# Kernel optimization log

Hardware: AMD Instinct MI355X
Metric: run time of the kernel (lower is better)

The kernel has to match this reference:

```python
import jax, jax.numpy as jnp
import numpy as np

B, Z, H, T = 256, 512, 2048, 16
EPS = 1e-5

def _normalize(v):
    return v / (jnp.linalg.norm(v) + 1e-12)

def setup_inputs() -> dict:
    key = jax.random.key(0)
    ks = jax.random.split(key, 10)
    s = lambda fan: 1.0 / np.sqrt(fan)
    return {
        "z": jax.random.normal(ks[0], (B, Z), dtype=jnp.float32),
        "fc_w": jax.random.normal(ks[1], (Z, Z), dtype=jnp.float32) * s(Z),
        "fc_b": jnp.zeros((Z,), dtype=jnp.float32),
        "fc_u": _normalize(jax.random.normal(ks[2], (Z,), dtype=jnp.float32)),
        "w_ih": jax.random.normal(ks[3], (3 * H, Z), dtype=jnp.float32) * s(Z),
        "w_hh": jax.random.normal(ks[4], (3 * H, H), dtype=jnp.float32) * s(H),
        "b_ih": jnp.zeros((3 * H,), dtype=jnp.float32).at[H:2 * H].set(1.0),  # forget-gate bias init
        "b_hh": jnp.zeros((3 * H,), dtype=jnp.float32),
        "lin_w": jax.random.normal(ks[5], (Z, H), dtype=jnp.float32) * s(H),
        "lin_b": jnp.zeros((Z,), dtype=jnp.float32),
    }

def _spectral_norm(w, u):
    # one torch-style power iteration (u, v treated as constants)
    v = jax.lax.stop_gradient(_normalize(w.T @ u))
    u1 = jax.lax.stop_gradient(_normalize(w @ v))
    sigma = u1 @ (w @ v)
    return w / sigma

def reference(z, fc_w, fc_b, fc_u, w_ih, w_hh, b_ih, b_hh, lin_w, lin_b):
    # spectral-norm linear: h0 = z @ (W/sigma)^T + b
    w_sn = _spectral_norm(fc_w, fc_u)
    x0 = z @ w_sn.T + fc_b                      # [B, Z]
    h0 = jnp.zeros((B, H), dtype=z.dtype)       # initHidden

    def step(carry, _):
        x, h = carry
        gi = x @ w_ih.T + b_ih                  # [B, 3H]
        gh = h @ w_hh.T + b_hh                  # [B, 3H]
        i_r, i_z, i_n = jnp.split(gi, 3, axis=1)
        h_r, h_z, h_n = jnp.split(gh, 3, axis=1)
        r = jax.nn.sigmoid(i_r + h_r)
        u = jax.nn.sigmoid(i_z + h_z)
        n = jnp.tanh(i_n + r * h_n)
        h_new = (1.0 - u) * n + u * h
        x_new = h_new @ lin_w.T + lin_b         # [B, Z] fed back as next input
        return (x_new, h_new), x_new

    _, outs = jax.lax.scan(step, (x0, h0), None, length=T)  # [T, B, Z]

    # per-timestep BatchNorm1d(affine=False), training-mode batch stats
    mean = jnp.mean(outs, axis=1, keepdims=True)
    var = jnp.mean((outs - mean) ** 2, axis=1, keepdims=True)
    y = (outs - mean) / jnp.sqrt(var + EPS)     # [T, B, Z]

    y = jnp.transpose(y, (1, 0, 2))             # [B, T, Z]
    return y.reshape(-1, Z)                     # [B*T, Z]
```

## Files before the change

kernel.cpp:

```cpp
#include <hip/hip_runtime.h>
#include <hip/hip_bf16.h>
#include <cstdint>
#include <cstddef>

#define B_  256
#define Z_  512
#define H_  2048
#define T_  16
#define H3_ 6144

using short8  = __attribute__((ext_vector_type(8))) short;
using bf16x8  = __attribute__((ext_vector_type(8))) __bf16;
using f32x4   = __attribute__((ext_vector_type(4))) float;
using f32x16  = __attribute__((ext_vector_type(16))) float;

__device__ __forceinline__ f32x4 mfma_bf16(short8 a, short8 b, f32x4 c) {
  return __builtin_amdgcn_mfma_f32_16x16x32_bf16(
      __builtin_bit_cast(bf16x8, a), __builtin_bit_cast(bf16x8, b), c, 0, 0, 0);
}
__device__ __forceinline__ f32x16 mfma_bf16_32(short8 a, short8 b, f32x16 c) {
  return __builtin_amdgcn_mfma_f32_32x32x16_bf16(
      __builtin_bit_cast(bf16x8, a), __builtin_bit_cast(bf16x8, b), c, 0, 0, 0);
}

__device__ __forceinline__ unsigned short f2bf(float f) {
  unsigned int u = __builtin_bit_cast(unsigned int, f);
  u = (u + 0x7FFFu + ((u >> 16) & 1u)) >> 16;
  return (unsigned short)u;
}

__device__ __forceinline__ float sigmoidf_(float x) { return 1.0f / (1.0f + __expf(-x)); }

__device__ __forceinline__ int swz(int row, int chunk) {
  return row * 64 + ((chunk ^ (row & 7)) << 3);
}

__global__ __launch_bounds__(512, 1) void gru_step7(
    const unsigned short* __restrict__ A, int K,
    const unsigned short* __restrict__ Wr,
    const unsigned short* __restrict__ Wz,
    const unsigned short* __restrict__ Wn,
    const unsigned short* __restrict__ Whn,
    const float* __restrict__ cr, const float* __restrict__ cz,
    const float* __restrict__ cn, const float* __restrict__ chn,
    float hn_scale,
    const float* __restrict__ h_old,
    float* __restrict__ h_new,
    unsigned short* __restrict__ h_hist)
{
  __shared__ __align__(16) unsigned short sbuf[2][12288];
  __shared__ float red[6][4096];
  float* LDSf = (float*)sbuf;
  const int bid = blockIdx.x, tid = threadIdx.x;
  const int xcd = bid & 7, rst = bid >> 3;
  const int m_idx = rst & 3, gg = rst >> 2;
  const int grp = gg * 8 + xcd;
  const int m0 = m_idx * 64;
  const int gh0 = grp * 32;
  const int wave = tid >> 6, lane = tid & 63;
  const int s4 = wave & 3, gp = wave >> 2;
  const int lh = lane >> 5, l31 = lane & 31;

  const int arow = tid >> 3, achk = tid & 7;
  const int wrow = tid >> 2, wc0 = (tid & 3) * 2;
  const unsigned short* wsrc =
      (wrow < 32) ? Wr : (wrow < 64) ? Wz : (wrow < 96) ? Wn : Whn;
  const size_t aoff = (size_t)(m0 + arow) * K + achk * 8;
  const size_t woff = (size_t)(gh0 + (wrow & 31)) * K + wc0 * 8;
  const int sa_d  = swz(arow, achk);
  const int sw_d0 = 4096 + swz(wrow, wc0 + 0);
  const int sw_d1 = 4096 + swz(wrow, wc0 + 1);

  uint4 Aa, Aw0, Aw1;
  uint4 Ba, Bw0, Bw1;

#define LDSET(a, w0, w1, k0)                               \
  {                                                        \
    const int kk_ = (k0);                                  \
    a  = *(const uint4*)(A    + aoff + kk_);               \
    w0 = *(const uint4*)(wsrc + woff + kk_);               \
    w1 = *(const uint4*)(wsrc + woff + kk_ + 8);           \
  }
#define STAGE(s, a, w0, w1)                                \
  {                                                        \
    unsigned short* b_ = sbuf[s];                          \
    *(uint4*)(b_ + sa_d)  = a;                             \
    *(uint4*)(b_ + sw_d0) = w0;                            \
    *(uint4*)(b_ + sw_d1) = w1;                            \
  }

  f32x16 a00 = {}, a01 = {}, a10 = {}, a11 = {};
  const int g0r = gp * 64, g1r = gp * 64 + 32;

#define COMP(sb)                                                           \
  {                                                                        \
    const unsigned short* b_ = sbuf[sb];                                   \
    const int ch = s4 * 2 + lh;                                            \
    short8 af0 = *(const short8*)(b_ + swz(l31, ch));                      \
    short8 af1 = *(const short8*)(b_ + swz(32 + l31, ch));                 \
    short8 wf0 = *(const short8*)(b_ + 4096 + swz(g0r + l31, ch));         \
    short8 wf1 = *(const short8*)(b_ + 4096 + swz(g1r + l31, ch));         \
    a00 = mfma_bf16_32(af0, wf0, a00);                                     \
    a01 = mfma_bf16_32(af0, wf1, a01);                                     \
    a10 = mfma_bf16_32(af1, wf0, a10);                                     \
    a11 = mfma_bf16_32(af1, wf1, a11);                                     \
  }

  const int nIter = K >> 6;
  LDSET(Aa, Aw0, Aw1, 0);
  LDSET(Ba, Bw0, Bw1, 64);
  for (int it = 0; it < nIter; it += 2) {
    STAGE(0, Aa, Aw0, Aw1);
    __syncthreads();
    { const int kn = (it + 2 < nIter) ? ((it + 2) << 6) : 0;
      LDSET(Aa, Aw0, Aw1, kn); }
    COMP(0);
    STAGE(1, Ba, Bw0, Bw1);
    __syncthreads();
    { const int kn = (it + 3 < nIter) ? ((it + 3) << 6) : 64;
      LDSET(Ba, Bw0, Bw1, kn); }
    COMP(1);
  }
#undef LDSET
#undef STAGE
#undef COMP

  __syncthreads();
  if (s4 != 0) {
    float* rp = red[(s4 - 1) * 2 + gp];
#pragma unroll
    for (int r = 0; r < 16; ++r) rp[(0 * 16 + r) * 64 + lane] = a00[r];
#pragma unroll
    for (int r = 0; r < 16; ++r) rp[(1 * 16 + r) * 64 + lane] = a01[r];
#pragma unroll
    for (int r = 0; r < 16; ++r) rp[(2 * 16 + r) * 64 + lane] = a10[r];
#pragma unroll
    for (int r = 0; r < 16; ++r) rp[(3 * 16 + r) * 64 + lane] = a11[r];
  }
  __syncthreads();
  if (s4 == 0) {
#pragma unroll
    for (int ss = 0; ss < 3; ++ss) {
      const float* rp = red[ss * 2 + gp];
#pragma unroll
      for (int r = 0; r < 16; ++r) a00[r] += rp[(0 * 16 + r) * 64 + lane];
#pragma unroll
      for (int r = 0; r < 16; ++r) a01[r] += rp[(1 * 16 + r) * 64 + lane];
#pragma unroll
      for (int r = 0; r < 16; ++r) a10[r] += rp[(2 * 16 + r) * 64 + lane];
#pragma unroll
      for (int r = 0; r < 16; ++r) a11[r] += rp[(3 * 16 + r) * 64 + lane];
    }
    const int gA = gp * 2, gB = gp * 2 + 1;
#pragma unroll
    for (int r = 0; r < 16; ++r) {
      const int trow = (r & 3) + 8 * (r >> 2) + 4 * lh;
      LDSf[(gA * 64 + trow     ) * 33 + l31] = a00[r];
      LDSf[(gB * 64 + trow     ) * 33 + l31] = a01[r];
      LDSf[(gA * 64 + 32 + trow) * 33 + l31] = a10[r];
      LDSf[(gB * 64 + 32 + trow) * 33 + l31] = a11[r];
    }
  }
  __syncthreads();
  {
    const int row = tid >> 3, c0 = (tid & 7) * 4;
    const int grow = m0 + row;
#pragma unroll
    for (int j = 0; j < 4; ++j) {
      const int col = c0 + j;
      const int gcol = gh0 + col;
      const float R   = sigmoidf_(LDSf[(0 * 64 + row) * 33 + col] + cr[gcol]);
      const float U   = sigmoidf_(LDSf[(1 * 64 + row) * 33 + col] + cz[gcol]);
      const float HNv = hn_scale * LDSf[(3 * 64 + row) * 33 + col] + chn[gcol];
      const float Nv  = tanhf(LDSf[(2 * 64 + row) * 33 + col] + cn[gcol] + R * HNv);
      const float ho  = h_old ? h_old[(size_t)grow * H_ + gcol] : 0.0f;
      const float hv  = (1.0f - U) * Nv + U * ho;
      h_new[(size_t)grow * H_ + gcol]  = hv;
      h_hist[(size_t)grow * H_ + gcol] = f2bf(hv);
    }
  }
}

__global__ __launch_bounds__(512) void gemm128_wsum(
    const unsigned short* __restrict__ w_ih_q,
    const unsigned short* __restrict__ lin_wT_q,
    const float* __restrict__ w_hh,
    unsigned short* __restrict__ Wsum_r,
    unsigned short* __restrict__ Wsum_z,
    unsigned short* __restrict__ Wn_c)
{
  __shared__ __align__(16) unsigned short sA[2][8192];
  __shared__ __align__(16) unsigned short sB[2][8192];
  const int g = blockIdx.y >> 4, nj = blockIdx.y & 15;
  const unsigned short* Aq = w_ih_q + (size_t)g * H_ * Z_;
  const float* adds = (g < 2) ? (w_hh + (size_t)g * H_ * H_) : nullptr;
  unsigned short* outw = (g == 0) ? Wsum_r : (g == 1) ? Wsum_z : Wn_c;
  const int K = Z_;
  const int m0 = blockIdx.x * 128, n0 = nj * 128;
  const int tid = threadIdx.x;
  const int wave = tid >> 6, lane = tid & 63;
  const int wr = wave & 1, wc = wave >> 1;
  const int lh = lane >> 5, l31 = lane & 31;
  const int srow = tid >> 2, sc0 = (tid & 3) * 2;
  const size_t aoff = (size_t)(m0 + srow) * K + sc0 * 8;
  const size_t boff = (size_t)(n0 + srow) * K + sc0 * 8;
  const int sd0 = swz(srow, sc0), sd1 = swz(srow, sc0 + 1);
  f32x16 acc0 = {}, acc1 = {};
  uint4 A0, A1, B0, B1, C0, C1, D0, D1;
#define LD(a0, a1, b0, b1, k0)                              \
  { const int kk_ = (k0);                                   \
    a0 = *(const uint4*)(Aq + aoff + kk_);                  \
    a1 = *(const uint4*)(Aq + aoff + kk_ + 8);              \
    b0 = *(const uint4*)(lin_wT_q + boff + kk_);            \
    b1 = *(const uint4*)(lin_wT_q + boff + kk_ + 8); }
#define ST(s, a0, a1, b0, b1)                               \
  { *(uint4*)(sA[s] + sd0) = a0; *(uint4*)(sA[s] + sd1) = a1; \
    *(uint4*)(sB[s] + sd0) = b0; *(uint4*)(sB[s] + sd1) = b1; }
#define CP(s)                                               \
  { _Pragma("unroll")                                       \
    for (int ks = 0; ks < 4; ++ks) {                        \
      const int ch = ks * 2 + lh;                           \
      short8 af0 = *(const short8*)(sA[s] + swz(wr * 64 + l31, ch));      \
      short8 af1 = *(const short8*)(sA[s] + swz(wr * 64 + 32 + l31, ch)); \
      short8 bf  = *(const short8*)(sB[s] + swz(wc * 32 + l31, ch));      \
      acc0 = mfma_bf16_32(af0, bf, acc0);                   \
      acc1 = mfma_bf16_32(af1, bf, acc1); } }
  const int nIter = K >> 6;
  LD(A0, A1, B0, B1, 0);
  LD(C0, C1, D0, D1, 64);
  for (int it = 0; it < nIter; it += 2) {
    ST(0, A0, A1, B0, B1);
    __syncthreads();
    { const int kn = (it + 2 < nIter) ? ((it + 2) << 6) : 0; LD(A0, A1, B0, B1, kn); }
    CP(0);
    ST(1, C0, C1, D0, D1);
    __syncthreads();
    { const int kn = (it + 3 < nIter) ? ((it + 3) << 6) : 64; LD(C0, C1, D0, D1, kn); }
    CP(1);
  }
#undef LD
#undef ST
#undef CP
#pragma unroll
  for (int i = 0; i < 2; ++i) {
    const f32x16 a = i ? acc1 : acc0;
#pragma unroll
    for (int r = 0; r < 16; ++r) {
      const int row = m0 + wr * 64 + i * 32 + (r & 3) + 8 * (r >> 2) + 4 * lh;
      const int col = n0 + wc * 32 + l31;
      float val = a[r];
      if (adds) val += adds[(size_t)row * H_ + col];
      outw[(size_t)row * H_ + col] = f2bf(val);
    }
  }
}

__global__ __launch_bounds__(256) void gemm_bt(
    const unsigned short* __restrict__ A,
    const unsigned short* __restrict__ Bw,
    int K,
    const float* __restrict__ addsrc, int add_ld,
    const float* __restrict__ bias,
    const float* __restrict__ scale_ptr,
    unsigned short* __restrict__ out_bf,
    float* __restrict__ out_f, int ldo)
{
  __shared__ unsigned short sA[32 * 64];
  __shared__ unsigned short sB[64 * 64];
  const int tid  = threadIdx.x;
  const int m0   = blockIdx.x * 32, n0 = blockIdx.y * 64;
  const int wave = tid >> 6, lane = tid & 63;
  const int wr = wave & 1, wc = wave >> 1;
  const int q = lane >> 4, c16 = lane & 15;
  const int lr = tid >> 3, lc8 = tid & 7;
  f32x4 acc0 = {}, acc1 = {};
  const size_t rowA  = (size_t)(m0 + lr) * K;
  const size_t rowB0 = (size_t)(n0 + lr) * K;
  const size_t rowB1 = (size_t)(n0 + 32 + lr) * K;
  for (int k0 = 0; k0 < K; k0 += 64) {
    const int gc = k0 + lc8 * 8;
    uint4 ra  = *(const uint4*)(A  + rowA  + gc);
    uint4 rb0 = *(const uint4*)(Bw + rowB0 + gc);
    uint4 rb1 = *(const uint4*)(Bw + rowB1 + gc);
    __syncthreads();
    *(uint4*)(sA + swz(lr, lc8))      = ra;
    *(uint4*)(sB + swz(lr, lc8))      = rb0;
    *(uint4*)(sB + swz(32 + lr, lc8)) = rb1;
    __syncthreads();
#pragma unroll
    for (int kk = 0; kk < 2; ++kk) {
      const int arow = wr * 16 + c16;
      short8 af = *(const short8*)(sA + swz(arow, kk * 4 + q));
      const int brow = wc * 32 + c16;
      short8 b0 = *(const short8*)(sB + swz(brow, kk * 4 + q));
      acc0 = mfma_bf16(af, b0, acc0);
      short8 b1 = *(const short8*)(sB + swz(brow + 16, kk * 4 + q));
      acc1 = mfma_bf16(af, b1, acc1);
    }
  }
  const float scale = scale_ptr ? *scale_ptr : 1.0f;
#pragma unroll
  for (int cf = 0; cf < 2; ++cf) {
    f32x4 a = cf ? acc1 : acc0;
#pragma unroll
    for (int v = 0; v < 4; ++v) {
      const int row = m0 + wr * 16 + q * 4 + v;
      const int col = n0 + wc * 32 + cf * 16 + c16;
      float val = a[v] * scale;
      if (addsrc) val += addsrc[(size_t)row * add_ld + col];
      if (bias)   val += bias[col];
      if (out_f)  out_f[(size_t)row * ldo + col] = val;
      if (out_bf) out_bf[(size_t)row * ldo + col] = f2bf(val);
    }
  }
}

__global__ __launch_bounds__(256) void gemm_bt64(
    const unsigned short* __restrict__ A,
    const unsigned short* __restrict__ Bw,
    int K,
    const float* __restrict__ addsrc, int add_ld,
    const float* __restrict__ bias,
    unsigned short* __restrict__ out_bf,
    float* __restrict__ out_f, int ldo)
{
  __shared__ unsigned short sA[64 * 64];
  __shared__ unsigned short sB[64 * 64];
  const int tid  = threadIdx.x;
  const int m0   = blockIdx.x * 64, n0 = blockIdx.y * 64;
  const int wave = tid >> 6, lane = tid & 63;
  const int wr = wave & 1, wc = wave >> 1;
  const int q = lane >> 4, c16 = lane & 15;
  const int lr = tid >> 3, lc8 = tid & 7;
  f32x4 acc[2][2] = {};
  const size_t aoff = (size_t)(m0 + lr) * K;
  const size_t boff = (size_t)(n0 + lr) * K;
  const size_t s32  = (size_t)32 * K;

  uint4 ra0, ra1, rb0, rb1;
  auto LOAD = [&](int k0) {
    const int gc = k0 + lc8 * 8;
    ra0 = *(const uint4*)(A  + aoff + gc);
    ra1 = *(const uint4*)(A  + aoff + s32 + gc);
    rb0 = *(const uint4*)(Bw + boff + gc);
    rb1 = *(const uint4*)(Bw + boff + s32 + gc);
  };

  const int nIter = K >> 6;
  LOAD(0);
  for (int it = 0; it < nIter; ++it) {
    __syncthreads();
    *(uint4*)(sA + swz(lr, lc8))      = ra0;
    *(uint4*)(sA + swz(lr + 32, lc8)) = ra1;
    *(uint4*)(sB + swz(lr, lc8))      = rb0;
    *(uint4*)(sB + swz(lr + 32, lc8)) = rb1;
    __syncthreads();
    if (it + 1 < nIter) LOAD((it + 1) << 6);
#pragma unroll
    for (int kk = 0; kk < 2; ++kk) {
      short8 af0 = *(const short8*)(sA + swz(wr * 32 + c16,      kk * 4 + q));
      short8 af1 = *(const short8*)(sA + swz(wr * 32 + 16 + c16, kk * 4 + q));
      short8 bf0 = *(const short8*)(sB + swz(wc * 32 + c16,      kk * 4 + q));
      short8 bf1 = *(const short8*)(sB + swz(wc * 32 + 16 + c16, kk * 4 + q));
      acc[0][0] = mfma_bf16(af0, bf0, acc[0][0]);
      acc[0][1] = mfma_bf16(af0, bf1, acc[0][1]);
      acc[1][0] = mfma_bf16(af1, bf0, acc[1][0]);
      acc[1][1] = mfma_bf16(af1, bf1, acc[1][1]);
    }
  }
#pragma unroll
  for (int i = 0; i < 2; ++i) {
#pragma unroll
    for (int j = 0; j < 2; ++j) {
#pragma unroll
      for (int v = 0; v < 4; ++v) {
        const int row = m0 + wr * 32 + i * 16 + q * 4 + v;
        const int col = n0 + wc * 32 + j * 16 + c16;
        float val = acc[i][j][v];
        if (addsrc) val += addsrc[(size_t)row * add_ld + col];
        if (bias)   val += bias[col];
        if (out_f)  out_f[(size_t)row * ldo + col] = val;
        if (out_bf) out_bf[(size_t)row * ldo + col] = f2bf(val);
      }
    }
  }
}

__global__ __launch_bounds__(256) void quant_all(
    const float* __restrict__ z, const float* __restrict__ fc_w,
    const float* __restrict__ w_ih, const float* __restrict__ w_hh,
    const float* __restrict__ lin_w,
    unsigned short* __restrict__ z_q, unsigned short* __restrict__ fc_w_q,
    unsigned short* __restrict__ w_ih_q, unsigned short* __restrict__ w_hhn_q,
    unsigned short* __restrict__ lin_w_q)
{
  const int i = blockIdx.x * 256 + threadIdx.x;
  if (i >= 2195456) return;
  const float4* src; ushort4* dst; int idx;
  if (i < 32768)        { src = (const float4*)z;     dst = (ushort4*)z_q;     idx = i; }
  else if (i < 98304)   { src = (const float4*)fc_w;  dst = (ushort4*)fc_w_q;  idx = i - 32768; }
  else if (i < 884736)  { src = (const float4*)w_ih;  dst = (ushort4*)w_ih_q;  idx = i - 98304; }
  else if (i < 1933312) { src = (const float4*)(w_hh + (size_t)2 * H_ * H_);
                          dst = (ushort4*)w_hhn_q;    idx = i - 884736; }
  else                  { src = (const float4*)lin_w; dst = (ushort4*)lin_w_q; idx = i - 1933312; }
  float4 v = src[idx];
  ushort4 o; o.x = f2bf(v.x); o.y = f2bf(v.y); o.z = f2bf(v.z); o.w = f2bf(v.w);
  dst[idx] = o;
}

__global__ __launch_bounds__(256) void transq(const float* __restrict__ s,
                                              unsigned short* __restrict__ d) {
  __shared__ float tile[32][33];
  const int tx = threadIdx.x & 31, ty = threadIdx.x >> 5;
  const int k0 = blockIdx.x * 32, z0 = blockIdx.y * 32;
#pragma unroll
  for (int j = 0; j < 4; ++j)
    tile[ty + j * 8][tx] = s[(size_t)(z0 + ty + j * 8) * H_ + k0 + tx];
  __syncthreads();
#pragma unroll
  for (int j = 0; j < 4; ++j)
    d[(size_t)(k0 + ty + j * 8) * Z_ + z0 + tx] = f2bf(tile[tx][ty + j * 8]);
}

__global__ void sigma1(const float* __restrict__ W, const float* __restrict__ u,
                       float* __restrict__ t1) {
  __shared__ float part[4][64];
  const int lane = threadIdx.x & 63, wv = threadIdx.x >> 6;
  const int col = blockIdx.x * 64 + lane;
  float s = 0.f;
  for (int r = wv * 128; r < wv * 128 + 128; ++r)
    s += W[(size_t)r * Z_ + col] * u[r];
  part[wv][lane] = s;
  __syncthreads();
  if (wv == 0)
    t1[col] = part[0][lane] + part[1][lane] + part[2][lane] + part[3][lane];
}

__global__ void sigma2(const float* __restrict__ W, const float* __restrict__ t1,
                       float* __restrict__ t2) {
  __shared__ float red[256];
  const int tid = threadIdx.x;
  float p = 0.f;
  for (int c = tid; c < Z_; c += 256) { float v = t1[c]; p += v * v; }
  red[tid] = p;
  __syncthreads();
  for (int s = 128; s > 0; s >>= 1) {
    if (tid < s) red[tid] += red[tid + s];
    __syncthreads();
  }
  const float invn = 1.0f / (sqrtf(red[0]) + 1e-12f);
  const int lane = tid & 63, wv = tid >> 6;
  const int row = blockIdx.x * 4 + wv;
  float s = 0.f;
  for (int c = lane; c < Z_; c += 64) s += W[(size_t)row * Z_ + c] * t1[c];
#pragma unroll
  for (int off = 32; off > 0; off >>= 1) s += __shfl_down(s, off);
  if (lane == 0) t2[row] = s * invn;
}

__global__ void sigma3(const float* __restrict__ t2, float* __restrict__ inv_sig) {
  __shared__ float red[256];
  int t = threadIdx.x;
  float v0 = t2[t], v1 = t2[t + 256];
  red[t] = v0 * v0 + v1 * v1;
  __syncthreads();
  for (int s = 128; s > 0; s >>= 1) {
    if (t < s) red[t] += red[t + s];
    __syncthreads();
  }
  if (t == 0) {
    float s2  = red[0];
    float sig = s2 / (sqrtf(s2) + 1e-12f);
    inv_sig[0] = 1.0f / sig;
  }
}

__global__ __launch_bounds__(256) void dots2_k(
    const float* __restrict__ w, const float* __restrict__ lb,
    const float* __restrict__ b_ih, const float* __restrict__ b_hh,
    float* __restrict__ c0r, float* __restrict__ c0z, float* __restrict__ c0n,
    float* __restrict__ c1r, float* __restrict__ c1z, float* __restrict__ c1n,
    float* __restrict__ chn)
{
  const int wave = threadIdx.x >> 6, lane = threadIdx.x & 63;
#pragma unroll
  for (int i = 0; i < 4; ++i) {
    int row = blockIdx.x * 16 + wave * 4 + i;
    float s = 0.f;
    for (int c = lane; c < Z_; c += 64) s += w[(size_t)row * Z_ + c] * lb[c];
#pragma unroll
    for (int off = 32; off > 0; off >>= 1) s += __shfl_down(s, off);
    if (lane == 0) {
      const int g = row >> 11, j = row & 2047;
      const float bi = b_ih[row], bh = b_hh[row];
      if (g == 0)      { c0r[j] = bi + bh; c1r[j] = bi + bh + s; }
      else if (g == 1) { c0z[j] = bi + bh; c1z[j] = bi + bh + s; }
      else             { c0n[j] = bi;      c1n[j] = bi + s;      chn[j] = bh; }
    }
  }
}

__global__ __launch_bounds__(256) void bn_k(const float* __restrict__ outs,
                                            float* __restrict__ y) {
  __shared__ float s_sum[4][64], s_sq[4][64], s_mean[64], s_inv[64];
  const int t = blockIdx.x, zb = blockIdx.y;
  const int zl = threadIdx.x & 63, bp = threadIdx.x >> 6;
  const int z = zb * 64 + zl;
  float sum = 0.f, sq = 0.f;
  for (int b = bp * 64; b < bp * 64 + 64; ++b) {
    float v = outs[(size_t)(t * 256 + b) * Z_ + z];
    sum += v; sq += v * v;
  }
  s_sum[bp][zl] = sum; s_sq[bp][zl] = sq;
  __syncthreads();
  if (bp == 0) {
    float S = s_sum[0][zl] + s_sum[1][zl] + s_sum[2][zl] + s_sum[3][zl];
    float Q = s_sq[0][zl] + s_sq[1][zl] + s_sq[2][zl] + s_sq[3][zl];
    float mean = S * (1.0f / 256.0f);
    float var  = Q * (1.0f / 256.0f) - mean * mean;
    s_mean[zl] = mean;
    s_inv[zl]  = rsqrtf(var + 1e-5f);
  }
  __syncthreads();
  const float mean = s_mean[zl], inv = s_inv[zl];
  for (int b = bp * 64; b < bp * 64 + 64; ++b) {
    float v = outs[(size_t)(t * 256 + b) * Z_ + z];
    y[(size_t)(b * T_ + t) * Z_ + z] = (v - mean) * inv;
  }
}

extern "C" void kernel_launch(void* const* d_in, const int* in_sizes, int n_in,
                              void* d_out, int out_size, void* d_ws, size_t ws_size,
                              hipStream_t stream) {
  const float* z     = (const float*)d_in[0];
  const float* fc_w  = (const float*)d_in[1];
  const float* fc_b  = (const float*)d_in[2];
  const float* fc_u  = (const float*)d_in[3];
  const float* w_ih  = (const float*)d_in[4];
  const float* w_hh  = (const float*)d_in[5];
  const float* b_ih  = (const float*)d_in[6];
  const float* b_hh  = (const float*)d_in[7];
  const float* lin_w = (const float*)d_in[8];
  const float* lin_b = (const float*)d_in[9];
  float* out = (float*)d_out;

  char* ws = (char*)d_ws;
  size_t off = 0;
  auto alloc = [&](size_t bytes) -> void* {
    off = (off + 255) & ~(size_t)255;
    void* p = ws + off;
    off += bytes;
    return p;
  };
  unsigned short* w_ih_q   = (unsigned short*)alloc((size_t)H3_ * Z_ * 2);
  unsigned short* w_hhn_q  = (unsigned short*)alloc((size_t)H_ * H_ * 2);
  unsigned short* lin_w_q  = (unsigned short*)alloc((size_t)Z_ * H_ * 2);
  unsigned short* lin_wT_q = (unsigned short*)alloc((size_t)Z_ * H_ * 2);
  unsigned short* fc_w_q   = (unsigned short*)alloc((size_t)Z_ * Z_ * 2);
  unsigned short* z_q      = (unsigned short*)alloc((size_t)B_ * Z_ * 2);
  unsigned short* x0_q     = (unsigned short*)alloc((size_t)B_ * Z_ * 2);
  unsigned short* Wsum_r   = (unsigned short*)alloc((size_t)H_ * H_ * 2);
  unsigned short* Wsum_z   = (unsigned short*)alloc((size_t)H_ * H_ * 2);
  unsigned short* Wn_c     = (unsigned short*)alloc((size_t)H_ * H_ * 2);
  unsigned short* Hhist    = (unsigned short*)alloc((size_t)T_ * B_ * H_ * 2);
  float* h_f32 = (float*)alloc((size_t)2 * B_ * H_ * 4);
  float* outs  = (float*)alloc((size_t)T_ * B_ * Z_ * 4);
  float* c0r = (float*)alloc(H_ * 4);
  float* c0z = (float*)alloc(H_ * 4);
  float* c0n = (float*)alloc(H_ * 4);
  float* c1r = (float*)alloc(H_ * 4);
  float* c1z = (float*)alloc(H_ * 4);
  float* c1n = (float*)alloc(H_ * 4);
  float* chn = (float*)alloc(H_ * 4);
  float* t1v = (float*)alloc(Z_ * 4);
  float* t2v = (float*)alloc(Z_ * 4);
  float* invsig = (float*)alloc(256);
  (void)in_sizes; (void)n_in; (void)out_size; (void)ws_size;

  quant_all<<<dim3((2195456 + 255) / 256), 256, 0, stream>>>(
      z, fc_w, w_ih, w_hh, lin_w, z_q, fc_w_q, w_ih_q, w_hhn_q, lin_w_q);
  transq<<<dim3(64, 16), 256, 0, stream>>>(lin_w, lin_wT_q);
  sigma1<<<8, 256, 0, stream>>>(fc_w, fc_u, t1v);
  sigma2<<<128, 256, 0, stream>>>(fc_w, t1v, t2v);
  sigma3<<<1, 256, 0, stream>>>(t2v, invsig);
  dots2_k<<<384, 256, 0, stream>>>(w_ih, lin_b, b_ih, b_hh,
                                   c0r, c0z, c0n, c1r, c1z, c1n, chn);

  gemm_bt<<<dim3(B_ / 32, Z_ / 64), 256, 0, stream>>>(
      z_q, fc_w_q, Z_, nullptr, 0, fc_b, invsig, x0_q, nullptr, Z_);

  gemm128_wsum<<<dim3(H_ / 128, 48), 512, 0, stream>>>(
      w_ih_q, lin_wT_q, w_hh, Wsum_r, Wsum_z, Wn_c);

  for (int t = 0; t < T_; ++t) {
    if (t == 0) {
      gru_step7<<<256, 512, 0, stream>>>(
          x0_q, Z_,
          w_ih_q, w_ih_q + (size_t)H_ * Z_, w_ih_q + (size_t)2 * H_ * Z_,
          w_ih_q ,
          c0r, c0z, c0n, chn, 0.0f, nullptr, h_f32, Hhist);
    } else {
      gru_step7<<<256, 512, 0, stream>>>(
          Hhist + (size_t)(t - 1) * B_ * H_, H_,
          Wsum_r, Wsum_z, Wn_c, w_hhn_q,
          c1r, c1z, c1n, chn, 1.0f,
          h_f32 + (size_t)((t - 1) & 1) * B_ * H_,
          h_f32 + (size_t)(t & 1) * B_ * H_,
          Hhist + (size_t)t * B_ * H_);
    }
  }

  gemm_bt64<<<dim3(T_ * B_ / 64, Z_ / 64), 256, 0, stream>>>(
      Hhist, lin_w_q, H_, nullptr, 0, lin_b, nullptr, outs, Z_);

  bn_k<<<dim3(T_, Z_ / 64), 256, 0, stream>>>(outs, out);
}
```

Measured before the change: 411.4 us.

## Use direct global-to-LDS loads in GRU step and XCD-swizzle GEMM tiles

The per-step GRU kernel now loads A and weight tiles with global_load_lds straight into swizzled LDS. This replaces the register-staged double buffer with a single-sync-per-iteration pipeline, cutting VGPR traffic and LDS store instructions on the recurrent critical path. The W-sum precompute GEMM moves from a 128x128 32x32-MFMA kernel to a shared 64x64 core with an XCD-aware block remap, and the output GEMM gets the same remap for L2 locality. The new load path relies on the swizzle being built into the per-lane global addresses. A single barrier per iteration may expose load latency or cause overwrite races.

Result: slower. 530.0 us (+28.8%).

```diff
diff --git a/kernel.cpp b/kernel.cpp
--- a/kernel.cpp
+++ b/kernel.cpp
@@ -35,7 +35,13 @@
   return row * 64 + ((chunk ^ (row & 7)) << 3);
 }
 
-__global__ __launch_bounds__(512, 1) void gru_step7(
+__device__ __forceinline__ void gload16(const unsigned short* g, unsigned short* l) {
+  __builtin_amdgcn_global_load_lds(
+      (const __attribute__((address_space(1))) unsigned int*)g,
+      (__attribute__((address_space(3))) unsigned int*)l, 16, 0, 0);
+}
+
+__global__ __launch_bounds__(512, 1) void gru_step8(
     const unsigned short* __restrict__ A, int K,
     const unsigned short* __restrict__ Wr,
     const unsigned short* __restrict__ Wz,
@@ -61,37 +67,31 @@
   const int s4 = wave & 3, gp = wave >> 2;
   const int lh = lane >> 5, l31 = lane & 31;
 
-  const int arow = tid >> 3, achk = tid & 7;
-  const int wrow = tid >> 2, wc0 = (tid & 3) * 2;
+  const int lrow8 = lane >> 3;
+  const int csw = ((lane & 7) ^ lrow8) << 3;
+  const int arow = wave * 8 + lrow8;
+  const unsigned short* gA = A + (size_t)(m0 + arow) * K + csw;
+  const int wv2 = wave >> 1;
   const unsigned short* wsrc =
-      (wrow < 32) ? Wr : (wrow < 64) ? Wz : (wrow < 96) ? Wn : Whn;
-  const size_t aoff = (size_t)(m0 + arow) * K + achk * 8;
-  const size_t woff = (size_t)(gh0 + (wrow & 31)) * K + wc0 * 8;
-  const int sa_d  = swz(arow, achk);
-  const int sw_d0 = 4096 + swz(wrow, wc0 + 0);
-  const int sw_d1 = 4096 + swz(wrow, wc0 + 1);
-
-  uint4 Aa, Aw0, Aw1;
-  uint4 Ba, Bw0, Bw1;
-
-#define LDSET(a, w0, w1, k0)                               \
-  {                                                        \
-    const int kk_ = (k0);                                  \
-    a  = *(const uint4*)(A    + aoff + kk_);               \
-    w0 = *(const uint4*)(wsrc + woff + kk_);               \
-    w1 = *(const uint4*)(wsrc + woff + kk_ + 8);           \
-  }
-#define STAGE(s, a, w0, w1)                                \
+      (wv2 == 0) ? Wr : (wv2 == 1) ? Wz : (wv2 == 2) ? Wn : Whn;
+  const int wrow0 = (wave * 16 + lrow8) & 31;
+  const int wrow1 = (wave * 16 + 8 + lrow8) & 31;
+  const unsigned short* gW0 = wsrc + (size_t)(gh0 + wrow0) * K + csw;
+  const unsigned short* gW1 = wsrc + (size_t)(gh0 + wrow1) * K + csw;
+  const int ldsA  = wave * 512;
+  const int ldsW0 = 4096 + wave * 1024;
+  const int ldsW1 = 4096 + wave * 1024 + 512;
+
+  f32x16 a00 = {}, a01 = {}, a10 = {}, a11 = {};
+  const int g0r = gp * 64, g1r = gp * 64 + 32;
+
+#define ISSUE(s, k0)                                       \
   {                                                        \
     unsigned short* b_ = sbuf[s];                          \
-    *(uint4*)(b_ + sa_d)  = a;                             \
-    *(uint4*)(b_ + sw_d0) = w0;                            \
-    *(uint4*)(b_ + sw_d1) = w1;                            \
-  }
-
-  f32x16 a00 = {}, a01 = {}, a10 = {}, a11 = {};
-  const int g0r = gp * 64, g1r = gp * 64 + 32;
-
+    gload16(gA  + (k0), b_ + ldsA);                        \
+    gload16(gW0 + (k0), b_ + ldsW0);                       \
+    gload16(gW1 + (k0), b_ + ldsW1);                       \
+  }
 #define COMP(sb)                                                           \
   {                                                                        \
     const unsigned short* b_ = sbuf[sb];                                   \
@@ -107,25 +107,16 @@
   }
 
   const int nIter = K >> 6;
-  LDSET(Aa, Aw0, Aw1, 0);
-  LDSET(Ba, Bw0, Bw1, 64);
-  for (int it = 0; it < nIter; it += 2) {
-    STAGE(0, Aa, Aw0, Aw1);
-    __syncthreads();
-    { const int kn = (it + 2 < nIter) ? ((it + 2) << 6) : 0;
-      LDSET(Aa, Aw0, Aw1, kn); }
-    COMP(0);
-    STAGE(1, Ba, Bw0, Bw1);
-    __syncthreads();
-    { const int kn = (it + 3 < nIter) ? ((it + 3) << 6) : 64;
-      LDSET(Ba, Bw0, Bw1, kn); }
-    COMP(1);
-  }
-#undef LDSET
-#undef STAGE
+  ISSUE(0, 0);
+  __syncthreads();
+  for (int it = 0; it < nIter; ++it) {
+    if (it + 1 < nIter) ISSUE((it + 1) & 1, (it + 1) << 6);
+    COMP(it & 1);
+    __syncthreads();
+  }
+#undef ISSUE
 #undef COMP
 
-  __syncthreads();
   if (s4 != 0) {
     float* rp = red[(s4 - 1) * 2 + gp];
 #pragma unroll
@@ -151,14 +142,14 @@
 #pragma unroll
       for (int r = 0; r < 16; ++r) a11[r] += rp[(3 * 16 + r) * 64 + lane];
     }
-    const int gA = gp * 2, gB = gp * 2 + 1;
+    const int gA2 = gp * 2, gB2 = gp * 2 + 1;
 #pragma unroll
     for (int r = 0; r < 16; ++r) {
       const int trow = (r & 3) + 8 * (r >> 2) + 4 * lh;
-      LDSf[(gA * 64 + trow     ) * 33 + l31] = a00[r];
-      LDSf[(gB * 64 + trow     ) * 33 + l31] = a01[r];
-      LDSf[(gA * 64 + 32 + trow) * 33 + l31] = a10[r];
-      LDSf[(gB * 64 + 32 + trow) * 33 + l31] = a11[r];
+      LDSf[(gA2 * 64 + trow     ) * 33 + l31] = a00[r];
+      LDSf[(gB2 * 64 + trow     ) * 33 + l31] = a01[r];
+      LDSf[(gA2 * 64 + 32 + trow) * 33 + l31] = a10[r];
+      LDSf[(gB2 * 64 + 32 + trow) * 33 + l31] = a11[r];
     }
   }
   __syncthreads();
@@ -181,7 +172,77 @@
   }
 }
 
-__global__ __launch_bounds__(512) void gemm128_wsum(
+__device__ __forceinline__ void dev_gemm64core(
+    unsigned short* sA, unsigned short* sB,
+    const unsigned short* __restrict__ A,
+    const unsigned short* __restrict__ Bw,
+    int K,
+    const float* __restrict__ addsrc, int add_ld,
+    const float* __restrict__ bias,
+    unsigned short* __restrict__ out_bf,
+    float* __restrict__ out_f, int ldo, int mi, int ni)
+{
+  const int tid  = threadIdx.x;
+  const int m0   = mi * 64, n0 = ni * 64;
+  const int wave = tid >> 6, lane = tid & 63;
+  const int wr = wave & 1, wc = wave >> 1;
+  const int q = lane >> 4, c16 = lane & 15;
+  const int lr = tid >> 3, lc8 = tid & 7;
+  f32x4 acc[2][2] = {};
+  const size_t aoff = (size_t)(m0 + lr) * K;
+  const size_t boff = (size_t)(n0 + lr) * K;
+  const size_t s32  = (size_t)32 * K;
+
+  uint4 ra0, ra1, rb0, rb1;
+  auto LOAD = [&](int k0) {
+    const int gc = k0 + lc8 * 8;
+    ra0 = *(const uint4*)(A  + aoff + gc);
+    ra1 = *(const uint4*)(A  + aoff + s32 + gc);
+    rb0 = *(const uint4*)(Bw + boff + gc);
+    rb1 = *(const uint4*)(Bw + boff + s32 + gc);
+  };
+
+  const int nIter = K >> 6;
+  LOAD(0);
+  for (int it = 0; it < nIter; ++it) {
+    __syncthreads();
+    *(uint4*)(sA + swz(lr, lc8))      = ra0;
+    *(uint4*)(sA + swz(lr + 32, lc8)) = ra1;
+    *(uint4*)(sB + swz(lr, lc8))      = rb0;
+    *(uint4*)(sB + swz(lr + 32, lc8)) = rb1;
+    __syncthreads();
+    if (it + 1 < nIter) LOAD((it + 1) << 6);
+#pragma unroll
+    for (int kk = 0; kk < 2; ++kk) {
+      short8 af0 = *(const short8*)(sA + swz(wr * 32 + c16,      kk * 4 + q));
+      short8 af1 = *(const short8*)(sA + swz(wr * 32 + 16 + c16, kk * 4 + q));
+      short8 bf0 = *(const short8*)(sB + swz(wc * 32 + c16,      kk * 4 + q));
+      short8 bf1 = *(const short8*)(sB + swz(wc * 32 + 16 + c16, kk * 4 + q));
+      acc[0][0] = mfma_bf16(af0, bf0, acc[0][0]);
+      acc[0][1] = mfma_bf16(af0, bf1, acc[0][1]);
+      acc[1][0] = mfma_bf16(af1, bf0, acc[1][0]);
+      acc[1][1] = mfma_bf16(af1, bf1, acc[1][1]);
+    }
+  }
+#pragma unroll
+  for (int i = 0; i < 2; ++i) {
+#pragma unroll
+    for (int j = 0; j < 2; ++j) {
+#pragma unroll
+      for (int v = 0; v < 4; ++v) {
+        const int row = m0 + wr * 32 + i * 16 + q * 4 + v;
+        const int col = n0 + wc * 32 + j * 16 + c16;
+        float val = acc[i][j][v];
+        if (addsrc) val += addsrc[(size_t)row * add_ld + col];
+        if (bias)   val += bias[col];
+        if (out_f)  out_f[(size_t)row * ldo + col] = val;
+        if (out_bf) out_bf[(size_t)row * ldo + col] = f2bf(val);
+      }
+    }
+  }
+}
+
+__global__ __launch_bounds__(256) void gemm_wsum_swz(
     const unsigned short* __restrict__ w_ih_q,
     const unsigned short* __restrict__ lin_wT_q,
     const float* __restrict__ w_hh,
@@ -189,81 +250,37 @@
     unsigned short* __restrict__ Wsum_z,
     unsigned short* __restrict__ Wn_c)
 {
-  __shared__ __align__(16) unsigned short sA[2][8192];
-  __shared__ __align__(16) unsigned short sB[2][8192];
-  const int g = blockIdx.y >> 4, nj = blockIdx.y & 15;
-  const unsigned short* Aq = w_ih_q + (size_t)g * H_ * Z_;
+  __shared__ unsigned short sA[64 * 64];
+  __shared__ unsigned short sB[64 * 64];
+  const int j = (blockIdx.x & 7) * 384 + (blockIdx.x >> 3);
+  const int g = j >> 10, rem = j & 1023, mi = rem >> 5, nj = rem & 31;
   const float* adds = (g < 2) ? (w_hh + (size_t)g * H_ * H_) : nullptr;
   unsigned short* outw = (g == 0) ? Wsum_r : (g == 1) ? Wsum_z : Wn_c;
-  const int K = Z_;
-  const int m0 = blockIdx.x * 128, n0 = nj * 128;
-  const int tid = threadIdx.x;
-  const int wave = tid >> 6, lane = tid & 63;
-  const int wr = wave & 1, wc = wave >> 1;
-  const int lh = lane >> 5, l31 = lane & 31;
-  const int srow = tid >> 2, sc0 = (tid & 3) * 2;
-  const size_t aoff = (size_t)(m0 + srow) * K + sc0 * 8;
-  const size_t boff = (size_t)(n0 + srow) * K + sc0 * 8;
-  const int sd0 = swz(srow, sc0), sd1 = swz(srow, sc0 + 1);
-  f32x16 acc0 = {}, acc1 = {};
-  uint4 A0, A1, B0, B1, C0, C1, D0, D1;
-#define LD(a0, a1, b0, b1, k0)                              \
-  { const int kk_ = (k0);                                   \
-    a0 = *(const uint4*)(Aq + aoff + kk_);                  \
-    a1 = *(const uint4*)(Aq + aoff + kk_ + 8);              \
-    b0 = *(const uint4*)(lin_wT_q + boff + kk_);            \
-    b1 = *(const uint4*)(lin_wT_q + boff + kk_ + 8); }
-#define ST(s, a0, a1, b0, b1)                               \
-  { *(uint4*)(sA[s] + sd0) = a0; *(uint4*)(sA[s] + sd1) = a1; \
-    *(uint4*)(sB[s] + sd0) = b0; *(uint4*)(sB[s] + sd1) = b1; }
-#define CP(s)                                               \
-  { _Pragma("unroll")                                       \
-    for (int ks = 0; ks < 4; ++ks) {                        \
-      const int ch = ks * 2 + lh;                           \
-      short8 af0 = *(const short8*)(sA[s] + swz(wr * 64 + l31, ch));      \
-      short8 af1 = *(const short8*)(sA[s] + swz(wr * 64 + 32 + l31, ch)); \
-      short8 bf  = *(const short8*)(sB[s] + swz(wc * 32 + l31, ch));      \
-      acc0 = mfma_bf16_32(af0, bf, acc0);                   \
-      acc1 = mfma_bf16_32(af1, bf, acc1); } }
-  const int nIter = K >> 6;
-  LD(A0, A1, B0, B1, 0);
-  LD(C0, C1, D0, D1, 64);
-  for (int it = 0; it < nIter; it += 2) {
-    ST(0, A0, A1, B0, B1);
-    __syncthreads();
-    { const int kn = (it + 2 < nIter) ? ((it + 2) << 6) : 0; LD(A0, A1, B0, B1, kn); }
-    CP(0);
-    ST(1, C0, C1, D0, D1);
-    __syncthreads();
-    { const int kn = (it + 3 < nIter) ? ((it + 3) << 6) : 64; LD(C0, C1, D0, D1, kn); }
-    CP(1);
-  }
-#undef LD
-#undef ST
-#undef CP
-#pragma unroll
-  for (int i = 0; i < 2; ++i) {
-    const f32x16 a = i ? acc1 : acc0;
-#pragma unroll
-    for (int r = 0; r < 16; ++r) {
-      const int row = m0 + wr * 64 + i * 32 + (r & 3) + 8 * (r >> 2) + 4 * lh;
-      const int col = n0 + wc * 32 + l31;
-      float val = a[r];
-      if (adds) val += adds[(size_t)row * H_ + col];
-      outw[(size_t)row * H_ + col] = f2bf(val);
-    }
-  }
+  dev_gemm64core(sA, sB, w_ih_q + (size_t)g * H_ * Z_, lin_wT_q, Z_,
+                 adds, H_, nullptr, outw, nullptr, H_, mi, nj);
+}
+
+__global__ __launch_bounds__(256) void gemm_out_swz(
+    const unsigned short* __restrict__ A,
+    const unsigned short* __restrict__ Bw,
+    const float* __restrict__ bias,
+    float* __restrict__ out_f)
+{
+  __shared__ unsigned short sA[64 * 64];
+  __shared__ unsigned short sB[64 * 64];
+  const int j = (blockIdx.x & 7) * 64 + (blockIdx.x >> 3);
+  const int mi = j >> 3, nj = j & 7;
+  dev_gemm64core(sA, sB, A, Bw, H_, nullptr, 0, bias, nullptr, out_f, Z_,
+                 mi, nj);
 }
 
 __global__ __launch_bounds__(256) void gemm_bt(
     const unsigned short* __restrict__ A,
     const unsigned short* __restrict__ Bw,
     int K,
-    const float* __restrict__ addsrc, int add_ld,
     const float* __restrict__ bias,
     const float* __restrict__ scale_ptr,
-    unsigned short* __restrict__ out_bf,
-    float* __restrict__ out_f, int ldo)
+    unsigned short* __restrict__ out_bf, int ldo)
 {
   __shared__ unsigned short sA[32 * 64];
   __shared__ unsigned short sB[64 * 64];
@@ -307,81 +324,8 @@
       const int row = m0 + wr * 16 + q * 4 + v;
       const int col = n0 + wc * 32 + cf * 16 + c16;
       float val = a[v] * scale;
-      if (addsrc) val += addsrc[(size_t)row * add_ld + col];
       if (bias)   val += bias[col];
-      if (out_f)  out_f[(size_t)row * ldo + col] = val;
-      if (out_bf) out_bf[(size_t)row * ldo + col] = f2bf(val);
-    }
-  }
-}
-
-__global__ __launch_bounds__(256) void gemm_bt64(
-    const unsigned short* __restrict__ A,
-    const unsigned short* __restrict__ Bw,
-    int K,
-    const float* __restrict__ addsrc, int add_ld,
-    const float* __restrict__ bias,
-    unsigned short* __restrict__ out_bf,
-    float* __restrict__ out_f, int ldo)
-{
-  __shared__ unsigned short sA[64 * 64];
-  __shared__ unsigned short sB[64 * 64];
-  const int tid  = threadIdx.x;
-  const int m0   = blockIdx.x * 64, n0 = blockIdx.y * 64;
-  const int wave = tid >> 6, lane = tid & 63;
-  const int wr = wave & 1, wc = wave >> 1;
-  const int q = lane >> 4, c16 = lane & 15;
-  const int lr = tid >> 3, lc8 = tid & 7;
-  f32x4 acc[2][2] = {};
-  const size_t aoff = (size_t)(m0 + lr) * K;
-  const size_t boff = (size_t)(n0 + lr) * K;
-  const size_t s32  = (size_t)32 * K;
-
-  uint4 ra0, ra1, rb0, rb1;
-  auto LOAD = [&](int k0) {
-    const int gc = k0 + lc8 * 8;
-    ra0 = *(const uint4*)(A  + aoff + gc);
-    ra1 = *(const uint4*)(A  + aoff + s32 + gc);
-    rb0 = *(const uint4*)(Bw + boff + gc);
-    rb1 = *(const uint4*)(Bw + boff + s32 + gc);
-  };
-
-  const int nIter = K >> 6;
-  LOAD(0);
-  for (int it = 0; it < nIter; ++it) {
-    __syncthreads();
-    *(uint4*)(sA + swz(lr, lc8))      = ra0;
-    *(uint4*)(sA + swz(lr + 32, lc8)) = ra1;
-    *(uint4*)(sB + swz(lr, lc8))      = rb0;
-    *(uint4*)(sB + swz(lr + 32, lc8)) = rb1;
-    __syncthreads();
-    if (it + 1 < nIter) LOAD((it + 1) << 6);
-#pragma unroll
-    for (int kk = 0; kk < 2; ++kk) {
-      short8 af0 = *(const short8*)(sA + swz(wr * 32 + c16,      kk * 4 + q));
-      short8 af1 = *(const short8*)(sA + swz(wr * 32 + 16 + c16, kk * 4 + q));
-      short8 bf0 = *(const short8*)(sB + swz(wc * 32 + c16,      kk * 4 + q));
-      short8 bf1 = *(const short8*)(sB + swz(wc * 32 + 16 + c16, kk * 4 + q));
-      acc[0][0] = mfma_bf16(af0, bf0, acc[0][0]);
-      acc[0][1] = mfma_bf16(af0, bf1, acc[0][1]);
-      acc[1][0] = mfma_bf16(af1, bf0, acc[1][0]);
-      acc[1][1] = mfma_bf16(af1, bf1, acc[1][1]);
-    }
-  }
-#pragma unroll
-  for (int i = 0; i < 2; ++i) {
-#pragma unroll
-    for (int j = 0; j < 2; ++j) {
-#pragma unroll
-      for (int v = 0; v < 4; ++v) {
-        const int row = m0 + wr * 32 + i * 16 + q * 4 + v;
-        const int col = n0 + wc * 32 + j * 16 + c16;
-        float val = acc[i][j][v];
-        if (addsrc) val += addsrc[(size_t)row * add_ld + col];
-        if (bias)   val += bias[col];
-        if (out_f)  out_f[(size_t)row * ldo + col] = val;
-        if (out_bf) out_bf[(size_t)row * ldo + col] = f2bf(val);
-      }
+      out_bf[(size_t)row * ldo + col] = f2bf(val);
     }
   }
 }
@@ -587,20 +531,20 @@
                                    c0r, c0z, c0n, c1r, c1z, c1n, chn);
 
   gemm_bt<<<dim3(B_ / 32, Z_ / 64), 256, 0, stream>>>(
-      z_q, fc_w_q, Z_, nullptr, 0, fc_b, invsig, x0_q, nullptr, Z_);
-
-  gemm128_wsum<<<dim3(H_ / 128, 48), 512, 0, stream>>>(
+      z_q, fc_w_q, Z_, fc_b, invsig, x0_q, Z_);
+
+  gemm_wsum_swz<<<3072, 256, 0, stream>>>(
       w_ih_q, lin_wT_q, w_hh, Wsum_r, Wsum_z, Wn_c);
 
   for (int t = 0; t < T_; ++t) {
     if (t == 0) {
-      gru_step7<<<256, 512, 0, stream>>>(
+      gru_step8<<<256, 512, 0, stream>>>(
           x0_q, Z_,
           w_ih_q, w_ih_q + (size_t)H_ * Z_, w_ih_q + (size_t)2 * H_ * Z_,
           w_ih_q ,
           c0r, c0z, c0n, chn, 0.0f, nullptr, h_f32, Hhist);
     } else {
-      gru_step7<<<256, 512, 0, stream>>>(
+      gru_step8<<<256, 512, 0, stream>>>(
           Hhist + (size_t)(t - 1) * B_ * H_, H_,
           Wsum_r, Wsum_z, Wn_c, w_hhn_q,
           c1r, c1z, c1n, chn, 1.0f,
@@ -610,8 +554,7 @@
     }
   }
 
-  gemm_bt64<<<dim3(T_ * B_ / 64, Z_ / 64), 256, 0, stream>>>(
-      Hhist, lin_w_q, H_, nullptr, 0, lin_b, nullptr, outs, Z_);
+  gemm_out_swz<<<512, 256, 0, stream>>>(Hhist, lin_w_q, lin_b, outs);
 
   bn_k<<<dim3(T_, Z_ / 64), 256, 0, stream>>>(outs, out);
 }
```
